# Kernel optimization log

Measured on AMD Instinct MI355X. Metric: run time of the kernel, lower is better.

Reference implementation:

```python
import jax, jax.numpy as jnp
import numpy as np

PH, PW = 7, 7            # pooled_height, pooled_width
SCALE = 0.0625           # spatial_scale = 1/16


def setup_inputs() -> dict:
    key = jax.random.key(0)
    k1, k2, k3, k4 = jax.random.split(key, 4)
    N, C, H, W, R = 4, 512, 64, 64, 2000
    features = jax.random.normal(k1, (N, C, H, W), jnp.float32)
    # rois: (batch_idx, x1, y1, x2, y2) in image coords (image = H/SCALE x W/SCALE)
    b = jax.random.randint(k2, (R,), 0, N).astype(jnp.float32)
    xs = jnp.sort(jax.random.uniform(k3, (R, 2), jnp.float32, 0.0, W / SCALE - 1.0), axis=1)
    ys = jnp.sort(jax.random.uniform(k4, (R, 2), jnp.float32, 0.0, H / SCALE - 1.0), axis=1)
    rois = jnp.stack([b, xs[:, 0], ys[:, 0], xs[:, 1], ys[:, 1]], axis=1)
    return {"features": features, "rois": rois}


def _roi_pool(features, rois):
    # split ROI into PH x PW bins with floor/ceil boundaries, max-pool each bin.
    N, C, H, W = features.shape
    # Max spatial extent of one bin: ceil(H/PH)+1 rows; +2 is a safe static bound.
    Kh = int(np.ceil(H / PH)) + 2
    Kw = int(np.ceil(W / PW)) + 2

    def per_roi(roi):
        b = roi[0].astype(jnp.int32)
        x1 = jnp.round(roi[1] * SCALE).astype(jnp.int32)
        y1 = jnp.round(roi[2] * SCALE).astype(jnp.int32)
        x2 = jnp.round(roi[3] * SCALE).astype(jnp.int32)
        y2 = jnp.round(roi[4] * SCALE).astype(jnp.int32)
        roi_w = jnp.maximum(x2 - x1 + 1, 1).astype(jnp.float32)
        roi_h = jnp.maximum(y2 - y1 + 1, 1).astype(jnp.float32)
        bin_h = roi_h / PH
        bin_w = roi_w / PW
        ih = jnp.arange(PH, dtype=jnp.float32)
        iw = jnp.arange(PW, dtype=jnp.float32)
        hstart = jnp.clip(jnp.floor(ih * bin_h).astype(jnp.int32) + y1, 0, H)        # [PH]
        hend = jnp.clip(jnp.ceil((ih + 1.0) * bin_h).astype(jnp.int32) + y1, 0, H)   # [PH]
        wstart = jnp.clip(jnp.floor(iw * bin_w).astype(jnp.int32) + x1, 0, W)        # [PW]
        wend = jnp.clip(jnp.ceil((iw + 1.0) * bin_w).astype(jnp.int32) + x1, 0, W)   # [PW]
        # Fixed-size windows per bin, with validity masks
        hidx = hstart[:, None] + jnp.arange(Kh)[None, :]          # [PH, Kh]
        hval = hidx < hend[:, None]
        hidx = jnp.clip(hidx, 0, H - 1)
        widx = wstart[:, None] + jnp.arange(Kw)[None, :]          # [PW, Kw]
        wval = widx < wend[:, None]
        widx = jnp.clip(widx, 0, W - 1)
        fmap = features[b]                                        # [C, H, W]
        gh = fmap[:, hidx, :]                                     # [C, PH, Kh, W]
        win = gh[:, :, :, widx]                                   # [C, PH, Kh, PW, Kw]
        valid = hval[:, :, None, None] & wval[None, None, :, :]   # [PH, Kh, PW, Kw]
        mx = jnp.where(valid[None], win, -jnp.inf).max(axis=(2, 4))  # [C, PH, PW]
        empty = (hend <= hstart)[:, None] | (wend <= wstart)[None, :]  # [PH, PW]
        return jnp.where(empty[None], jnp.zeros_like(mx), mx)

    # Sequential map over ROIs keeps peak memory at ~one ROI's window buffer.
    return jax.lax.map(per_roi, rois)  # [R, C, PH, PW]


def reference(features, rois):
    return _roi_pool(features, rois)
```

## Files before the change

kernel.cpp:

```cpp
#include <hip/hip_runtime.h>
#include <math.h>
#include <float.h>

#define PH 7
#define RLEN 32

#define C7 9586981LL

__device__ __forceinline__ long long round24(long long v) {
    if (v == 0) return 0;
    int L = 64 - __clzll((unsigned long long)v);
    int sh = L - 24;
    if (sh <= 0) return v;
    long long rem  = v & ((1LL << sh) - 1);
    long long base = v >> sh;
    long long half = 1LL << (sh - 1);
    if (rem > half || (rem == half && (base & 1))) base++;
    return base << sh;
}
__device__ __forceinline__ long long bin_q26(int roi) {
    return round24((long long)roi * C7);
}
__device__ __forceinline__ int floor_k(long long b26, int k) {
    long long v = round24((long long)k * b26);
    return (int)(v >> 26);
}
__device__ __forceinline__ int ceil_k(long long b26, int k) {
    long long v = round24((long long)k * b26);
    return (int)((v + ((1LL << 26) - 1)) >> 26);
}

__global__ void roi_bounds_kernel(const float* __restrict__ rois,
                                  int* __restrict__ wsbuf, int R) {
    int r = blockIdx.x * blockDim.x + threadIdx.x;
    if (r >= R) return;
    const int H = 64, W = 64;
    const float* roi = rois + r * 5;
    int b  = (int)roi[0];
    int x1 = (int)rintf(roi[1] * 0.0625f);
    int y1 = (int)rintf(roi[2] * 0.0625f);
    int x2 = (int)rintf(roi[3] * 0.0625f);
    int y2 = (int)rintf(roi[4] * 0.0625f);

    int roi_w = max(x2 - x1 + 1, 1);
    int roi_h = max(y2 - y1 + 1, 1);
    long long bh = bin_q26(roi_h);
    long long bw = bin_q26(roi_w);

    int* o = wsbuf + r * RLEN;
    o[0] = b;
    int ws0 = 64, we6 = 0;
    #pragma unroll
    for (int i = 0; i < PH; ++i) {
        int hs = min(max(y1 + floor_k(bh, i),     0), H);
        int he = min(max(y1 + ceil_k (bh, i + 1), 0), H);
        int wst = min(max(x1 + floor_k(bw, i),     0), W);
        int wen = min(max(x1 + ceil_k (bw, i + 1), 0), W);
        o[1 + i]  = hs;
        o[8 + i]  = he;
        o[16 + i] = wst;
        o[23 + i] = wen;
        if (i == 0) ws0 = wst;
        if (i == 6) we6 = wen;
    }
    int qs = ws0 >> 2;
    int qe = (we6 + 3) >> 2;
    o[15] = qs | (max(qe, qs) << 8);
}

__device__ __forceinline__ float4 max4(float4 a, float4 b) {
    float4 r;
    r.x = fmaxf(a.x, b.x); r.y = fmaxf(a.y, b.y);
    r.z = fmaxf(a.z, b.z); r.w = fmaxf(a.w, b.w);
    return r;
}

__global__ __launch_bounds__(256) void roipool_main(
        const float* __restrict__ features,
        const int* __restrict__ wsbuf,
        float* __restrict__ out) {
    __shared__ float cmA[4][8][68];
    __shared__ float cmB[4][8][68];

    int r    = blockIdx.x >> 4;
    int cg   = blockIdx.x & 15;
    int wv   = threadIdx.x >> 6;
    int lane = threadIdx.x & 63;
    int chsub = lane >> 3;
    int cq8   = lane & 7;
    int c0   = (cg << 5) + (wv << 3);

    const int* B = wsbuf + r * RLEN;
    int b   = B[0];
    int qpk = B[15];
    int qs  = qpk & 255;
    int qe  = qpk >> 8;
    bool dual = (qe - qs) > 8;

    const float4* f4 = (const float4*)features;
    int cbase = ((b << 9) + c0 + chsub) << 10;
    int qabs0 = qs + cq8;
    int qabs1 = qs + 8 + cq8;
    bool m0 = qabs0 < qe;
    bool m1 = qabs1 < qe;
    int qc1 = min(qabs1, 15);

    int ech = (lane * 9363) >> 16;
    int epw = lane - ech * 7;
    int ews = B[16 + epw];
    int ewe = B[23 + epw];
    bool eact = lane < 56;
    const float* erowA = cmA[wv][ech & 7];
    const float* erowB = cmB[wv][ech & 7];
    float vals[PH];
    int phs = 0, phe = 0;

    const float4 NEG4 = make_float4(-FLT_MAX, -FLT_MAX, -FLT_MAX, -FLT_MAX);
    float4 last0 = NEG4, last1 = NEG4;
    int last_h = -100;

    if (!dual) {
        #pragma unroll
        for (int ph = 0; ph < PH; ++ph) {
            int hs = B[1 + ph], he = B[8 + ph];
            float (*cw)[68] = (ph & 1) ? cmB[wv] : cmA[wv];
            if (m0 && he > hs) {
                bool reuse = (hs == last_h);
                float4 a0 = reuse ? last0 : NEG4;
                int h0 = hs + (reuse ? 1 : 0);
                int nbody = he - h0 - 1;
                int idx = cbase + (h0 << 4) + qabs0;
                while (nbody >= 4) {
                    float4 v0 = f4[idx];
                    float4 v1 = f4[idx + 16];
                    float4 v2 = f4[idx + 32];
                    float4 v3 = f4[idx + 48];
                    a0 = max4(a0, max4(max4(v0, v1), max4(v2, v3)));
                    idx += 64; nbody -= 4;
                }
                if (nbody >= 2) {
                    float4 v0 = f4[idx];
                    float4 v1 = f4[idx + 16];
                    a0 = max4(a0, max4(v0, v1));
                    idx += 32; nbody -= 2;
                }
                if (nbody >= 1) a0 = max4(a0, f4[idx]);
                if (he - 1 >= h0) {
                    last0 = f4[cbase + ((he - 1) << 4) + qabs0];
                    a0 = max4(a0, last0);
                }
                last_h = he - 1;
                *(float4*)&cw[chsub][qabs0 << 2] = a0;
            }
            if (ph > 0) {
                const float* er = (ph & 1) ? erowA : erowB;
                float m = -FLT_MAX;
                int w = ews;
                for (; w + 2 <= ewe; w += 2)
                    m = fmaxf(fmaxf(m, er[w]), er[w + 1]);
                if (w < ewe) m = fmaxf(m, er[w]);
                vals[ph - 1] = ((phe <= phs) || (ewe <= ews)) ? 0.0f : m;
            }
            phs = hs; phe = he;
        }
    } else {
        #pragma unroll
        for (int ph = 0; ph < PH; ++ph) {
            int hs = B[1 + ph], he = B[8 + ph];
            float (*cw)[68] = (ph & 1) ? cmB[wv] : cmA[wv];
            if (he > hs) {
                bool reuse = (hs == last_h);
                float4 a0 = reuse ? last0 : NEG4;
                float4 a1 = reuse ? last1 : NEG4;
                int h0 = hs + (reuse ? 1 : 0);
                int nbody = he - h0 - 1;
                int idx = cbase + (h0 << 4);
                while (nbody >= 2) {
                    float4 v00 = f4[idx + qabs0];
                    float4 v01 = f4[idx + qc1];
                    float4 v10 = f4[idx + 16 + qabs0];
                    float4 v11 = f4[idx + 16 + qc1];
                    a0 = max4(a0, max4(v00, v10));
                    a1 = max4(a1, max4(v01, v11));
                    idx += 32; nbody -= 2;
                }
                if (nbody >= 1) {
                    a0 = max4(a0, f4[idx + qabs0]);
                    a1 = max4(a1, f4[idx + qc1]);
                }
                if (he - 1 >= h0) {
                    int fin = cbase + ((he - 1) << 4);
                    last0 = f4[fin + qabs0];
                    last1 = f4[fin + qc1];
                    a0 = max4(a0, last0);
                    a1 = max4(a1, last1);
                }
                last_h = he - 1;
                *(float4*)&cw[chsub][qabs0 << 2] = a0;
                if (m1) *(float4*)&cw[chsub][qabs1 << 2] = a1;
            }
            if (ph > 0) {
                const float* er = (ph & 1) ? erowA : erowB;
                float m = -FLT_MAX;
                int w = ews;
                for (; w + 2 <= ewe; w += 2)
                    m = fmaxf(fmaxf(m, er[w]), er[w + 1]);
                if (w < ewe) m = fmaxf(m, er[w]);
                vals[ph - 1] = ((phe <= phs) || (ewe <= ews)) ? 0.0f : m;
            }
            phs = hs; phe = he;
        }
    }
    {
        float m = -FLT_MAX;
        int w = ews;
        for (; w + 2 <= ewe; w += 2)
            m = fmaxf(fmaxf(m, erowA[w]), erowA[w + 1]);
        if (w < ewe) m = fmaxf(m, erowA[w]);
        vals[PH - 1] = ((phe <= phs) || (ewe <= ews)) ? 0.0f : m;
    }

    float* stage = (float*)cmA[wv];
    if (eact) {
        #pragma unroll
        for (int ph = 0; ph < PH; ++ph)
            stage[ech * 49 + ph * 7 + epw] = vals[ph];
    }
    size_t obase = ((size_t)(r << 9) + c0) * 49;
    #pragma unroll
    for (int it = 0; it < 7; ++it) {
        int f = (it << 6) + lane;
        if (f < 392) out[obase + f] = stage[f];
    }
}

extern "C" void kernel_launch(void* const* d_in, const int* in_sizes, int n_in,
                              void* d_out, int out_size, void* d_ws, size_t ws_size,
                              hipStream_t stream) {
    const float* features = (const float*)d_in[0];
    const float* rois     = (const float*)d_in[1];
    float* out = (float*)d_out;
    int* wsbuf = (int*)d_ws;

    int R = in_sizes[1] / 5;

    roi_bounds_kernel<<<(R + 255) / 256, 256, 0, stream>>>(rois, wsbuf, R);
    roipool_main<<<R * 16, 256, 0, stream>>>(features, wsbuf, out);
}
```

Baseline: 193.2 us.

## Add narrow-ROI path mapping 16 channels per wave with 4 quads each

Adds a specialized path for ROIs whose width spans at most 4 float4 quads. Each wave then covers 16 channels with 4 lanes per channel instead of 8 channels with 8 lanes, so half the blocks exit early and far fewer lanes sit masked off. Shared memory becomes one unified buffer with separate A/B layouts for the two paths. The trade-off is extra registers and branch divergence between paths, and blocks with cg>=8 launch only to exit immediately.

```diff
diff --git a/kernel.cpp b/kernel.cpp
--- a/kernel.cpp
+++ b/kernel.cpp
@@ -79,43 +79,152 @@
         const float* __restrict__ features,
         const int* __restrict__ wsbuf,
         float* __restrict__ out) {
-    __shared__ float cmA[4][8][68];
-    __shared__ float cmB[4][8][68];
+    __shared__ float U[4][1088];
 
     int r    = blockIdx.x >> 4;
     int cg   = blockIdx.x & 15;
     int wv   = threadIdx.x >> 6;
     int lane = threadIdx.x & 63;
-    int chsub = lane >> 3;
-    int cq8   = lane & 7;
-    int c0   = (cg << 5) + (wv << 3);
 
     const int* B = wsbuf + r * RLEN;
     int b   = B[0];
     int qpk = B[15];
     int qs  = qpk & 255;
     int qe  = qpk >> 8;
-    bool dual = (qe - qs) > 8;
+    int nq  = qe - qs;
 
     const float4* f4 = (const float4*)features;
+    const float4 NEG4 = make_float4(-FLT_MAX, -FLT_MAX, -FLT_MAX, -FLT_MAX);
+
+    int ech = (lane * 9363) >> 16;
+    int epw = lane - ech * 7;
+    int ews = B[16 + epw];
+    int ewe = B[23 + epw];
+    bool eact = lane < 56;
+
+    float* bufA = U[wv];
+
+    if (nq <= 4) {
+        if (cg >= 8) return;
+        int c0    = (cg << 6) + (wv << 4);
+        int chsub = lane >> 2;
+        int cq4   = lane & 3;
+        int qabs  = qs + cq4;
+        bool m0   = qabs < qe;
+        int cbase = ((b << 9) + c0 + chsub) << 10;
+        float* bufB = U[wv] + 320;
+
+        int ewsr = ews - (qs << 2);
+        int ewer = ewe - (qs << 2);
+        const float* erA0 = bufA + (ech & 7) * 20;
+        const float* erA1 = bufA + (8 + (ech & 7)) * 20;
+        const float* erB0 = bufB + (ech & 7) * 20;
+        const float* erB1 = bufB + (8 + (ech & 7)) * 20;
+        float vals0[PH], vals1[PH];
+        int phs = 0, phe = 0;
+        float4 last0 = NEG4;
+        int last_h = -100;
+
+        #pragma unroll
+        for (int ph = 0; ph < PH; ++ph) {
+            int hs = B[1 + ph], he = B[8 + ph];
+            float* cw = (ph & 1) ? bufB : bufA;
+            if (m0 && he > hs) {
+                bool reuse = (hs == last_h);
+                float4 a0 = reuse ? last0 : NEG4;
+                int h0 = hs + (reuse ? 1 : 0);
+                int nbody = he - h0 - 1;
+                int idx = cbase + (h0 << 4) + qabs;
+                while (nbody >= 4) {
+                    float4 v0 = f4[idx];
+                    float4 v1 = f4[idx + 16];
+                    float4 v2 = f4[idx + 32];
+                    float4 v3 = f4[idx + 48];
+                    a0 = max4(a0, max4(max4(v0, v1), max4(v2, v3)));
+                    idx += 64; nbody -= 4;
+                }
+                if (nbody >= 2) {
+                    float4 v0 = f4[idx];
+                    float4 v1 = f4[idx + 16];
+                    a0 = max4(a0, max4(v0, v1));
+                    idx += 32; nbody -= 2;
+                }
+                if (nbody >= 1) a0 = max4(a0, f4[idx]);
+                if (he - 1 >= h0) {
+                    last0 = f4[cbase + ((he - 1) << 4) + qabs];
+                    a0 = max4(a0, last0);
+                }
+                last_h = he - 1;
+                *(float4*)&cw[chsub * 20 + (cq4 << 2)] = a0;
+            }
+            if (ph > 0) {
+                const float* e0 = (ph & 1) ? erA0 : erB0;
+                const float* e1 = (ph & 1) ? erA1 : erB1;
+                bool empty = (phe <= phs) || (ewe <= ews);
+                float m = -FLT_MAX;
+                int w = ewsr;
+                for (; w + 2 <= ewer; w += 2)
+                    m = fmaxf(fmaxf(m, e0[w]), e0[w + 1]);
+                if (w < ewer) m = fmaxf(m, e0[w]);
+                vals0[ph - 1] = empty ? 0.0f : m;
+                m = -FLT_MAX;
+                w = ewsr;
+                for (; w + 2 <= ewer; w += 2)
+                    m = fmaxf(fmaxf(m, e1[w]), e1[w + 1]);
+                if (w < ewer) m = fmaxf(m, e1[w]);
+                vals1[ph - 1] = empty ? 0.0f : m;
+            }
+            phs = hs; phe = he;
+        }
+        {
+            bool empty = (phe <= phs) || (ewe <= ews);
+            float m = -FLT_MAX;
+            int w = ewsr;
+            for (; w + 2 <= ewer; w += 2)
+                m = fmaxf(fmaxf(m, erA0[w]), erA0[w + 1]);
+            if (w < ewer) m = fmaxf(m, erA0[w]);
+            vals0[PH - 1] = empty ? 0.0f : m;
+            m = -FLT_MAX;
+            w = ewsr;
+            for (; w + 2 <= ewer; w += 2)
+                m = fmaxf(fmaxf(m, erA1[w]), erA1[w + 1]);
+            if (w < ewer) m = fmaxf(m, erA1[w]);
+            vals1[PH - 1] = empty ? 0.0f : m;
+        }
+        float* stage = U[wv];
+        if (eact) {
+            #pragma unroll
+            for (int ph = 0; ph < PH; ++ph) {
+                stage[ech * 49 + ph * 7 + epw] = vals0[ph];
+                stage[(8 + ech) * 49 + ph * 7 + epw] = vals1[ph];
+            }
+        }
+        size_t obase = ((size_t)(r << 9) + c0) * 49;
+        #pragma unroll
+        for (int it = 0; it < 13; ++it) {
+            int f = (it << 6) + lane;
+            if (f < 784) out[obase + f] = stage[f];
+        }
+        return;
+    }
+
+    int c0    = (cg << 5) + (wv << 3);
+    int chsub = lane >> 3;
+    int cq8   = lane & 7;
+    bool dual = nq > 8;
     int cbase = ((b << 9) + c0 + chsub) << 10;
     int qabs0 = qs + cq8;
     int qabs1 = qs + 8 + cq8;
     bool m0 = qabs0 < qe;
     bool m1 = qabs1 < qe;
     int qc1 = min(qabs1, 15);
-
-    int ech = (lane * 9363) >> 16;
-    int epw = lane - ech * 7;
-    int ews = B[16 + epw];
-    int ewe = B[23 + epw];
-    bool eact = lane < 56;
-    const float* erowA = cmA[wv][ech & 7];
-    const float* erowB = cmB[wv][ech & 7];
+    float* bufB = U[wv] + 544;
+
+    const float* erowA = bufA + (ech & 7) * 68;
+    const float* erowB = bufB + (ech & 7) * 68;
     float vals[PH];
     int phs = 0, phe = 0;
 
-    const float4 NEG4 = make_float4(-FLT_MAX, -FLT_MAX, -FLT_MAX, -FLT_MAX);
     float4 last0 = NEG4, last1 = NEG4;
     int last_h = -100;
 
@@ -123,7 +232,7 @@
         #pragma unroll
         for (int ph = 0; ph < PH; ++ph) {
             int hs = B[1 + ph], he = B[8 + ph];
-            float (*cw)[68] = (ph & 1) ? cmB[wv] : cmA[wv];
+            float* cw = (ph & 1) ? bufB : bufA;
             if (m0 && he > hs) {
                 bool reuse = (hs == last_h);
                 float4 a0 = reuse ? last0 : NEG4;
@@ -150,7 +259,7 @@
                     a0 = max4(a0, last0);
                 }
                 last_h = he - 1;
-                *(float4*)&cw[chsub][qabs0 << 2] = a0;
+                *(float4*)&cw[chsub * 68 + (qabs0 << 2)] = a0;
             }
             if (ph > 0) {
                 const float* er = (ph & 1) ? erowA : erowB;
@@ -167,7 +276,7 @@
         #pragma unroll
         for (int ph = 0; ph < PH; ++ph) {
             int hs = B[1 + ph], he = B[8 + ph];
-            float (*cw)[68] = (ph & 1) ? cmB[wv] : cmA[wv];
+            float* cw = (ph & 1) ? bufB : bufA;
             if (he > hs) {
                 bool reuse = (hs == last_h);
                 float4 a0 = reuse ? last0 : NEG4;
@@ -196,8 +305,8 @@
                     a1 = max4(a1, last1);
                 }
                 last_h = he - 1;
-                *(float4*)&cw[chsub][qabs0 << 2] = a0;
-                if (m1) *(float4*)&cw[chsub][qabs1 << 2] = a1;
+                *(float4*)&cw[chsub * 68 + (qabs0 << 2)] = a0;
+                if (m1) *(float4*)&cw[chsub * 68 + (qabs1 << 2)] = a1;
             }
             if (ph > 0) {
                 const float* er = (ph & 1) ? erowA : erowB;
@@ -220,7 +329,7 @@
         vals[PH - 1] = ((phe <= phs) || (ewe <= ews)) ? 0.0f : m;
     }
 
-    float* stage = (float*)cmA[wv];
+    float* stage = U[wv];
     if (eact) {
         #pragma unroll
         for (int ph = 0; ph < PH; ++ph)
```

Measured after the change: 281.5 us. 45.7% more time.

## Sort ROIs by batch index to improve feature-map cache locality

Applied to the files above, without the earlier changes.

Adds a single-wavefront kernel that counting-sorts ROI indices by batch index, and the main kernel now reads its ROI through this permutation. Blocks that run close together then tend to read the same image's feature map, which is meant to raise L2/MALL hit rates. The cost is an extra serial kernel launch over all ROIs and one indirect load per block. It also hardcodes four batch values (0-3).

```diff
diff --git a/kernel.cpp b/kernel.cpp
--- a/kernel.cpp
+++ b/kernel.cpp
@@ -68,6 +68,42 @@
     o[15] = qs | (max(qe, qs) << 8);
 }
 
+__global__ void roi_sort_kernel(const float* __restrict__ rois,
+                                int* __restrict__ order, int R) {
+    int lane = threadIdx.x;
+    int cnt0 = 0, cnt1 = 0, cnt2 = 0, cnt3 = 0;
+    for (int i = lane; i < R; i += 64) {
+        int b = (int)rois[i * 5];
+        cnt0 += (b == 0); cnt1 += (b == 1); cnt2 += (b == 2); cnt3 += (b == 3);
+    }
+    #pragma unroll
+    for (int s = 32; s > 0; s >>= 1) {
+        cnt0 += __shfl_down(cnt0, s);
+        cnt1 += __shfl_down(cnt1, s);
+        cnt2 += __shfl_down(cnt2, s);
+        cnt3 += __shfl_down(cnt3, s);
+    }
+    int off0 = 0, off1, off2, off3;
+    off1 = __shfl(cnt0, 0);
+    off2 = off1 + __shfl(cnt1, 0);
+    off3 = off2 + __shfl(cnt2, 0);
+    unsigned long long below = (1ull << lane) - 1ull;
+    for (int base = 0; base < R; base += 64) {
+        int i = base + lane;
+        int b = (i < R) ? (int)rois[i * 5] : -1;
+        unsigned long long m0 = __ballot(b == 0);
+        unsigned long long m1 = __ballot(b == 1);
+        unsigned long long m2 = __ballot(b == 2);
+        unsigned long long m3 = __ballot(b == 3);
+        if (b == 0) order[off0 + __popcll(m0 & below)] = i;
+        if (b == 1) order[off1 + __popcll(m1 & below)] = i;
+        if (b == 2) order[off2 + __popcll(m2 & below)] = i;
+        if (b == 3) order[off3 + __popcll(m3 & below)] = i;
+        off0 += __popcll(m0); off1 += __popcll(m1);
+        off2 += __popcll(m2); off3 += __popcll(m3);
+    }
+}
+
 __device__ __forceinline__ float4 max4(float4 a, float4 b) {
     float4 r;
     r.x = fmaxf(a.x, b.x); r.y = fmaxf(a.y, b.y);
@@ -78,11 +114,12 @@
 __global__ __launch_bounds__(256) void roipool_main(
         const float* __restrict__ features,
         const int* __restrict__ wsbuf,
+        const int* __restrict__ order,
         float* __restrict__ out) {
     __shared__ float cmA[4][8][68];
     __shared__ float cmB[4][8][68];
 
-    int r    = blockIdx.x >> 4;
+    int r    = order[blockIdx.x >> 4];
     int cg   = blockIdx.x & 15;
     int wv   = threadIdx.x >> 6;
     int lane = threadIdx.x & 63;
@@ -243,7 +280,9 @@
     int* wsbuf = (int*)d_ws;
 
     int R = in_sizes[1] / 5;
+    int* order = wsbuf + R * RLEN;
 
     roi_bounds_kernel<<<(R + 255) / 256, 256, 0, stream>>>(rois, wsbuf, R);
-    roipool_main<<<R * 16, 256, 0, stream>>>(features, wsbuf, out);
-}
+    roi_sort_kernel<<<1, 64, 0, stream>>>(rois, order, R);
+    roipool_main<<<R * 16, 256, 0, stream>>>(features, wsbuf, order, out);
+}
```

After: 179.5 us. 7.1% less time.
